# Kernel optimization log

Measured on AMD Instinct MI355X. Metric: run time of the kernel, lower is better.

Reference implementation:

```python
import jax, jax.numpy as jnp
import numpy as np

B, H, S, D = 4, 8, 4096, 64

def setup_inputs() -> dict:
    key = jax.random.key(0)
    kq, kk, kv = jax.random.split(key, 3)
    Q = jax.random.normal(kq, (B, H, S, D), dtype=jnp.float32)
    K = jax.random.normal(kk, (B, H, S, D), dtype=jnp.float32)
    V = jax.random.normal(kv, (B, H, S, D), dtype=jnp.float32)
    return {"Q": Q, "K": K, "V": V}

def reference(Q, K, V):
    scale = 1.0 / jnp.sqrt(jnp.float32(Q.shape[-1]))
    # scores: [B, H, S, S]
    scores = jnp.einsum('bhqd,bhkd->bhqk', Q, K) * scale
    attn = jax.nn.softmax(scores, axis=-1)
    # out: [B, H, S, D]
    return jnp.einsum('bhqk,bhkd->bhqd', attn, V)
```

## Files before the change

kernel.cpp:

```cpp
#include <hip/hip_runtime.h>
#include <hip/hip_bf16.h>

typedef float  f32x16 __attribute__((ext_vector_type(16)));
typedef __bf16 bf16x8 __attribute__((ext_vector_type(8)));
typedef __bf16 bf16x4 __attribute__((ext_vector_type(4)));
typedef __bf16 bf16x2 __attribute__((ext_vector_type(2)));
typedef int    i32x2v __attribute__((ext_vector_type(2)));
typedef int    i32x4v __attribute__((ext_vector_type(4)));

#define SEQ   4096
#define DDIM  64
#define KB    64
#define NT    (SEQ / KB)
#define TILEB 16384
#define WSNEED (32ull * NT * TILEB)
#define SCL   0.18033688011112042f
#define DEFT  16.0f

#if __has_builtin(__builtin_amdgcn_exp2f)
#define EXP2(x) __builtin_amdgcn_exp2f(x)
#else
#define EXP2(x) __expf((x) * 0.6931471805599453f)
#endif

__device__ __forceinline__ int swzb(int row) {
  return (row & 7) ^ ((row >> 3) & 3);
}

__device__ __forceinline__ void pswap32(int &x, int &y) {
#if __has_builtin(__builtin_amdgcn_permlane32_swap)
  i32x2v r = __builtin_amdgcn_permlane32_swap(x, y, false, false);
  x = r[0]; y = r[1];
#else
  asm volatile("v_permlane32_swap_b32 %0, %1" : "+v"(x), "+v"(y));
#endif
}

__device__ __forceinline__ void mfma_acc(f32x16 &acc, bf16x8 a, bf16x8 b) {
  asm("v_mfma_f32_32x32x16_bf16 %0, %1, %2, %0"
      : "+v"(acc) : "v"(a), "v"(b));
}
__device__ __forceinline__ f32x16 mfma_z(bf16x8 a, bf16x8 b) {
  f32x16 d;
  asm("v_mfma_f32_32x32x16_bf16 %0, %1, %2, 0"
      : "=v"(d) : "v"(a), "v"(b));
  return d;
}

__device__ __forceinline__ void gl_lds16(const char* g, char* l) {
  __builtin_amdgcn_global_load_lds(
      (const __attribute__((address_space(1))) void*)g,
      (__attribute__((address_space(3))) void*)l, 16, 0, 0);
}

__device__ __forceinline__ bf16x8 mkfrag(int a, int b, int c, int d) {
  i32x4v v; v[0] = a; v[1] = b; v[2] = c; v[3] = d;
  return __builtin_bit_cast(bf16x8, v);
}

__device__ __forceinline__ float max8(const f32x16& s, int o) {
  float m = fmaxf(fmaxf(s[o+0], s[o+1]), s[o+2]);
  m = fmaxf(fmaxf(m, s[o+3]), s[o+4]);
  m = fmaxf(fmaxf(m, s[o+5]), s[o+6]);
  return fmaxf(m, s[o+7]);
}

__global__ __launch_bounds__(256)
void prep(const float* __restrict__ Kg, const float* __restrict__ Vg,
          char* __restrict__ KVb)
{
  int i = blockIdx.x * 256 + threadIdx.x;
  if (i < (1 << 20)) {
    int row = i >> 3, s_in = i & 7;
    int bh = row >> 12, r = row & 4095, t = r >> 6, kv = r & 63;
    const float* src = Kg + (size_t)row * 64 + s_in * 8;
    float4 f0 = *(const float4*)(src);
    float4 f1 = *(const float4*)(src + 4);
    bf16x8 p;
    p[0] = (__bf16)f0.x; p[1] = (__bf16)f0.y; p[2] = (__bf16)f0.z; p[3] = (__bf16)f0.w;
    p[4] = (__bf16)f1.x; p[5] = (__bf16)f1.y; p[6] = (__bf16)f1.z; p[7] = (__bf16)f1.w;
    char* dst = KVb + (size_t)(bh * NT + t) * TILEB + kv * 128 + ((s_in ^ swzb(kv)) * 16);
    *(bf16x8*)dst = p;
  } else {
    int j = i - (1 << 20);
    int d = j & 63, rest = j >> 6;
    int kvg = rest & 7, t = (rest >> 3) & 63, bh = rest >> 9;
    const float* src = Vg + (size_t)bh * (SEQ * DDIM) + (t * 64 + kvg * 8) * 64 + d;
    bf16x8 p;
    #pragma unroll
    for (int jj = 0; jj < 8; ++jj) p[jj] = (__bf16)src[jj * 64];
    char* dst = KVb + (size_t)(bh * NT + t) * TILEB + 8192 + d * 128
              + ((kvg ^ swzb(d)) * 16);
    *(bf16x8*)dst = p;
  }
}

__global__ __launch_bounds__(512, 4)
void fattn(const float* __restrict__ Qg, const char* __restrict__ KVb,
           float* __restrict__ Og)
{
  __shared__ __align__(16) char smem[2 * TILEB];

  const int tid  = threadIdx.x;
  const int w    = tid >> 6;
  const int lane = tid & 63;
  const int q31  = lane & 31;
  const int h    = lane >> 5;

  int wg = (int)blockIdx.x;
  wg = (wg & 7) * 64 + (wg >> 3);
  const int bh = wg >> 4;
  const int qb = wg & 15;
  const size_t base = (size_t)bh * (SEQ * DDIM);
  const int qrow = qb * 256 + w * 32 + q31;

  bf16x8 aq[4];
  {
    const float* qp = Qg + base + (size_t)qrow * DDIM + 8 * h;
    #pragma unroll
    for (int c = 0; c < 4; ++c) {
      float4 f0 = *(const float4*)(qp + 16 * c);
      float4 f1 = *(const float4*)(qp + 16 * c + 4);
      aq[c][0] = (__bf16)(f0.x * SCL);
      aq[c][1] = (__bf16)(f0.y * SCL);
      aq[c][2] = (__bf16)(f0.z * SCL);
      aq[c][3] = (__bf16)(f0.w * SCL);
      aq[c][4] = (__bf16)(f1.x * SCL);
      aq[c][5] = (__bf16)(f1.y * SCL);
      aq[c][6] = (__bf16)(f1.z * SCL);
      aq[c][7] = (__bf16)(f1.w * SCL);
    }
  }

  const char* kvt = KVb + (size_t)bh * (NT * TILEB);
  const int stg   = w * 1024 + lane * 16;
  const int ldsw  = w * 1024;

  const int swr = swzb(q31) << 4;
  int kaddr[4];
  #pragma unroll
  for (int c = 0; c < 4; ++c)
    kaddr[c] = q31 * 128 + ((32 * c + 16 * h) ^ swr);

  f32x16 o0 = {}, o1 = {};
  float lsum = 0.f;
  int pk[2][8];

#if __has_builtin(__builtin_amdgcn_fdot2_f32_bf16)
  bf16x2 one2; one2[0] = (__bf16)1.0f; one2[1] = (__bf16)1.0f;
#endif

  auto softmax_pack = [&](f32x16& s0, f32x16& s1) {
    #pragma unroll
    for (int r = 0; r < 16; ++r) s0[r] = EXP2(s0[r]);
    #pragma unroll
    for (int r = 0; r < 16; ++r) s1[r] = EXP2(s1[r]);
    #pragma unroll
    for (int u = 0; u < 8; ++u) {
      bf16x2 p0; p0[0] = (__bf16)s0[2*u]; p0[1] = (__bf16)s0[2*u+1];
      pk[0][u] = __builtin_bit_cast(int, p0);
      bf16x2 p1; p1[0] = (__bf16)s1[2*u]; p1[1] = (__bf16)s1[2*u+1];
      pk[1][u] = __builtin_bit_cast(int, p1);
    }
#if __has_builtin(__builtin_amdgcn_fdot2_f32_bf16)
    float a0 = 0.f, a1 = 0.f, a2 = 0.f, a3 = 0.f;
    #pragma unroll
    for (int u = 0; u < 2; ++u) {
      a0 = __builtin_amdgcn_fdot2_f32_bf16(__builtin_bit_cast(bf16x2, pk[0][4*u+0]), one2, a0, false);
      a1 = __builtin_amdgcn_fdot2_f32_bf16(__builtin_bit_cast(bf16x2, pk[0][4*u+1]), one2, a1, false);
      a2 = __builtin_amdgcn_fdot2_f32_bf16(__builtin_bit_cast(bf16x2, pk[0][4*u+2]), one2, a2, false);
      a3 = __builtin_amdgcn_fdot2_f32_bf16(__builtin_bit_cast(bf16x2, pk[0][4*u+3]), one2, a3, false);
      a0 = __builtin_amdgcn_fdot2_f32_bf16(__builtin_bit_cast(bf16x2, pk[1][4*u+0]), one2, a0, false);
      a1 = __builtin_amdgcn_fdot2_f32_bf16(__builtin_bit_cast(bf16x2, pk[1][4*u+1]), one2, a1, false);
      a2 = __builtin_amdgcn_fdot2_f32_bf16(__builtin_bit_cast(bf16x2, pk[1][4*u+2]), one2, a2, false);
      a3 = __builtin_amdgcn_fdot2_f32_bf16(__builtin_bit_cast(bf16x2, pk[1][4*u+3]), one2, a3, false);
    }
    lsum += (a0 + a1) + (a2 + a3);
#else
    f32x16 ts = s0 + s1;
    lsum += ((((ts[0]+ts[1])+(ts[2]+ts[3])) + ((ts[4]+ts[5])+(ts[6]+ts[7])))
          +  (((ts[8]+ts[9])+(ts[10]+ts[11])) + ((ts[12]+ts[13])+(ts[14]+ts[15]))));
#endif
    #pragma unroll
    for (int m = 0; m < 2; ++m) {
      pswap32(pk[m][0], pk[m][2]);
      pswap32(pk[m][1], pk[m][3]);
      pswap32(pk[m][4], pk[m][6]);
      pswap32(pk[m][5], pk[m][7]);
    }
  };

  {
    const char* gp = kvt + stg;
    gl_lds16(gp,        smem + ldsw);
    gl_lds16(gp + 8192, smem + ldsw + 8192);
  }
  __syncthreads();

  for (int t = 0; t < NT; ++t) {
    const int cur  = (t & 1) << 14;
    const int nxtb = cur ^ TILEB;
    const bool more = (t + 1) < NT;

    if (more) {
      const char* gp = kvt + (size_t)(t + 1) * TILEB + stg;
      gl_lds16(gp,        smem + nxtb + ldsw);
      gl_lds16(gp + 8192, smem + nxtb + ldsw + 8192);
    }

    f32x16 s0, s1;
    __builtin_amdgcn_s_setprio(1);
    {
      bf16x8 k0 = *(const bf16x8*)(smem + cur + kaddr[0]);
      bf16x8 k1 = *(const bf16x8*)(smem + cur + kaddr[0] + 4096);
      s0 = mfma_z(k0, aq[0]);
      s1 = mfma_z(k1, aq[0]);
    }
    #pragma unroll
    for (int c = 1; c < 4; ++c) {
      bf16x8 k0 = *(const bf16x8*)(smem + cur + kaddr[c]);
      bf16x8 k1 = *(const bf16x8*)(smem + cur + kaddr[c] + 4096);
      mfma_acc(s0, k0, aq[c]);
      mfma_acc(s1, k1, aq[c]);
    }
    __builtin_amdgcn_s_setprio(0);

    softmax_pack(s0, s1);

    __builtin_amdgcn_s_setprio(1);
    #pragma unroll
    for (int c = 0; c < 4; ++c) {
      bf16x8 bp = mkfrag(pk[c>>1][(c&1)*4+0], pk[c>>1][(c&1)*4+1],
                         pk[c>>1][(c&1)*4+2], pk[c>>1][(c&1)*4+3]);
      bf16x8 v0 = *(const bf16x8*)(smem + cur + kaddr[c] + 8192);
      bf16x8 v1 = *(const bf16x8*)(smem + cur + kaddr[c] + 12288);
      mfma_acc(o0, v0, bp);
      mfma_acc(o1, v1, bp);
    }
    __builtin_amdgcn_s_setprio(0);

    __syncthreads();
  }

  float l = lsum + __shfl_xor(lsum, 32);
  float inv = 1.0f / l;
  float* op = Og + base + (size_t)qrow * DDIM + 4 * h;
  #pragma unroll
  for (int rg = 0; rg < 4; ++rg) {
    float4 st0 = { o0[4*rg+0]*inv, o0[4*rg+1]*inv, o0[4*rg+2]*inv, o0[4*rg+3]*inv };
    *(float4*)(op + 8*rg) = st0;
    float4 st1 = { o1[4*rg+0]*inv, o1[4*rg+1]*inv, o1[4*rg+2]*inv, o1[4*rg+3]*inv };
    *(float4*)(op + 8*rg + 32) = st1;
  }
}

__global__ __launch_bounds__(512)
void fattn_fb(const float* __restrict__ Qg, const float* __restrict__ Kg,
              const float* __restrict__ Vg, float* __restrict__ Og)
{
  __shared__ __align__(16) char smem[32768];
  const int tid  = threadIdx.x;
  const int w    = tid >> 6;
  const int lane = tid & 63;
  const int q31  = lane & 31;
  const int h    = lane >> 5;

  int wg = (int)blockIdx.x;
  wg = (wg & 7) * 64 + (wg >> 3);
  const int bh = wg >> 4;
  const int qb = wg & 15;
  const size_t base = (size_t)bh * (SEQ * DDIM);
  const int qrow = qb * 256 + w * 32 + q31;

  bf16x8 aq[4];
  {
    const float* qp = Qg + base + (size_t)qrow * DDIM + 8 * h;
    #pragma unroll
    for (int c = 0; c < 4; ++c) {
      float4 f0 = *(const float4*)(qp + 16 * c);
      float4 f1 = *(const float4*)(qp + 16 * c + 4);
      aq[c][0] = (__bf16)(f0.x * SCL); aq[c][1] = (__bf16)(f0.y * SCL);
      aq[c][2] = (__bf16)(f0.z * SCL); aq[c][3] = (__bf16)(f0.w * SCL);
      aq[c][4] = (__bf16)(f1.x * SCL); aq[c][5] = (__bf16)(f1.y * SCL);
      aq[c][6] = (__bf16)(f1.z * SCL); aq[c][7] = (__bf16)(f1.w * SCL);
    }
  }

  const int kvA = tid >> 4;
  const int dK  = (tid & 15) * 4;
  const int kw0 = ((kvA * 128 + dK * 2) ^ (swzb(kvA) << 4));
  const int kv0 = (tid >> 4) * 2;
  const int dV  = (tid & 15) * 4;
  int vw[4];
  #pragma unroll
  for (int qq = 0; qq < 4; ++qq)
    vw[qq] = 8192 + (((dV + qq) * 128 + kv0 * 2) ^ (swzb(dV + qq) << 4));
  const float* kptr = Kg + base + (size_t)kvA * DDIM + dK;
  const float* vptr = Vg + base + (size_t)kv0 * DDIM + dV;

  const int swr = swzb(q31) << 4;
  int kaddr[4];
  #pragma unroll
  for (int c = 0; c < 4; ++c)
    kaddr[c] = q31 * 128 + ((32 * c + 16 * h) ^ swr);

  f32x16 o0 = {}, o1 = {};
  float mrow = 0.f, lsum = 0.f;

  {
    float4 ka = *(const float4*)(kptr);
    float4 kb = *(const float4*)(kptr + 32 * DDIM);
    float4 va = *(const float4*)(vptr);
    float4 vb = *(const float4*)(vptr + DDIM);
    bf16x4 pa, pb;
    pa[0]=(__bf16)ka.x; pa[1]=(__bf16)ka.y; pa[2]=(__bf16)ka.z; pa[3]=(__bf16)ka.w;
    pb[0]=(__bf16)kb.x; pb[1]=(__bf16)kb.y; pb[2]=(__bf16)kb.z; pb[3]=(__bf16)kb.w;
    *(bf16x4*)(smem + kw0)            = pa;
    *(bf16x4*)(smem + kw0 + 32 * 128) = pb;
    float va4[4] = {va.x, va.y, va.z, va.w};
    float vb4[4] = {vb.x, vb.y, vb.z, vb.w};
    #pragma unroll
    for (int qq = 0; qq < 4; ++qq) {
      bf16x2 p; p[0] = (__bf16)va4[qq]; p[1] = (__bf16)vb4[qq];
      *(bf16x2*)(smem + vw[qq]) = p;
    }
  }

  int rbase = 0;
  for (int t = 0; t < NT; ++t) {
    __syncthreads();
    const bool more = (t + 1) < NT;
    const float* kpt = kptr + (size_t)(t + 1) * (KB * DDIM);
    const float* vpt = vptr + (size_t)(t + 1) * (KB * DDIM);
    float4 ka = {}, kb = {};
    if (more) { ka = *(const float4*)(kpt); kb = *(const float4*)(kpt + 32 * DDIM); }

    f32x16 s0 = {}, s1 = {};
    #pragma unroll
    for (int c = 0; c < 4; ++c) {
      bf16x8 k0 = *(const bf16x8*)(smem + rbase + kaddr[c]);
      bf16x8 k1 = *(const bf16x8*)(smem + rbase + kaddr[c] + 4096);
      s0 = __builtin_amdgcn_mfma_f32_32x32x16_bf16(k0, aq[c], s0, 0, 0, 0);
      s1 = __builtin_amdgcn_mfma_f32_32x32x16_bf16(k1, aq[c], s1, 0, 0, 0);
    }

    float4 va = {}, vb = {};
    if (more) { va = *(const float4*)(vpt); vb = *(const float4*)(vpt + DDIM); }

    float pm;
    {
      float m0 = max8(s0, 0), m1 = max8(s0, 8);
      float m2 = max8(s1, 0), m3 = max8(s1, 8);
      pm = fmaxf(fmaxf(m0, m1), fmaxf(m2, m3));
    }
    if (!__all(pm <= mrow + DEFT)) {
      float tm = fmaxf(pm, __shfl_xor(pm, 32));
      float mn = fmaxf(mrow, tm);
      float corr = EXP2(mrow - mn);
      o0 *= corr; o1 *= corr; lsum *= corr;
      mrow = mn;
    }
    #pragma unroll
    for (int r = 0; r < 16; ++r) s0[r] = EXP2(s0[r] - mrow);
    #pragma unroll
    for (int r = 0; r < 16; ++r) s1[r] = EXP2(s1[r] - mrow);
    f32x16 ts = s0 + s1;
    lsum += ((((ts[0]+ts[1])+(ts[2]+ts[3])) + ((ts[4]+ts[5])+(ts[6]+ts[7])))
          +  (((ts[8]+ts[9])+(ts[10]+ts[11])) + ((ts[12]+ts[13])+(ts[14]+ts[15]))));

    int pk[2][8];
    #pragma unroll
    for (int u = 0; u < 8; ++u) {
      bf16x2 p0; p0[0] = (__bf16)s0[2*u]; p0[1] = (__bf16)s0[2*u+1];
      pk[0][u] = __builtin_bit_cast(int, p0);
      bf16x2 p1; p1[0] = (__bf16)s1[2*u]; p1[1] = (__bf16)s1[2*u+1];
      pk[1][u] = __builtin_bit_cast(int, p1);
    }
    #pragma unroll
    for (int m = 0; m < 2; ++m) {
      pswap32(pk[m][0], pk[m][2]); pswap32(pk[m][1], pk[m][3]);
      pswap32(pk[m][4], pk[m][6]); pswap32(pk[m][5], pk[m][7]);
    }

    const int wb = rbase ^ 16384;
    if (more) {
      bf16x4 pa, pb;
      pa[0]=(__bf16)ka.x; pa[1]=(__bf16)ka.y; pa[2]=(__bf16)ka.z; pa[3]=(__bf16)ka.w;
      pb[0]=(__bf16)kb.x; pb[1]=(__bf16)kb.y; pb[2]=(__bf16)kb.z; pb[3]=(__bf16)kb.w;
      *(bf16x4*)(smem + wb + kw0)            = pa;
      *(bf16x4*)(smem + wb + kw0 + 32 * 128) = pb;
    }

    #pragma unroll
    for (int c = 0; c < 4; ++c) {
      bf16x8 bp = mkfrag(pk[c>>1][(c&1)*4+0], pk[c>>1][(c&1)*4+1],
                         pk[c>>1][(c&1)*4+2], pk[c>>1][(c&1)*4+3]);
      bf16x8 v0 = *(const bf16x8*)(smem + rbase + kaddr[c] + 8192);
      bf16x8 v1 = *(const bf16x8*)(smem + rbase + kaddr[c] + 12288);
      o0 = __builtin_amdgcn_mfma_f32_32x32x16_bf16(v0, bp, o0, 0, 0, 0);
      o1 = __builtin_amdgcn_mfma_f32_32x32x16_bf16(v1, bp, o1, 0, 0, 0);
    }

    if (more) {
      float va4[4] = {va.x, va.y, va.z, va.w};
      float vb4[4] = {vb.x, vb.y, vb.z, vb.w};
      #pragma unroll
      for (int qq = 0; qq < 4; ++qq) {
        bf16x2 p; p[0] = (__bf16)va4[qq]; p[1] = (__bf16)vb4[qq];
        *(bf16x2*)(smem + wb + vw[qq]) = p;
      }
    }
    rbase ^= 16384;
  }

  float l = lsum + __shfl_xor(lsum, 32);
  float inv = 1.0f / l;
  float* op = Og + base + (size_t)qrow * DDIM + 4 * h;
  #pragma unroll
  for (int rg = 0; rg < 4; ++rg) {
    float4 w0 = { o0[4*rg+0]*inv, o0[4*rg+1]*inv, o0[4*rg+2]*inv, o0[4*rg+3]*inv };
    *(float4*)(op + 8*rg) = w0;
    float4 w1 = { o1[4*rg+0]*inv, o1[4*rg+1]*inv, o1[4*rg+2]*inv, o1[4*rg+3]*inv };
    *(float4*)(op + 8*rg + 32) = w1;
  }
}

extern "C" void kernel_launch(void* const* d_in, const int* in_sizes, int n_in,
                              void* d_out, int out_size, void* d_ws, size_t ws_size,
                              hipStream_t stream) {
  const float* Q = (const float*)d_in[0];
  const float* K = (const float*)d_in[1];
  const float* V = (const float*)d_in[2];
  float* O = (float*)d_out;
  if (ws_size >= WSNEED) {
    prep<<<dim3(8192), dim3(256), 0, stream>>>(K, V, (char*)d_ws);
    fattn<<<dim3(512), dim3(512), 0, stream>>>(Q, (const char*)d_ws, O);
  } else {
    fattn_fb<<<dim3(512), dim3(512), 0, stream>>>(Q, K, V, O);
  }
}
```

Measured before the change: 155.6 us.

## Triple-buffer K/V tiles in LDS with two-ahead async prefetch

Moves the K/V staging from double to triple buffering. Each loop iteration now prefetches the tile two steps ahead, and the full __syncthreads is replaced by a partial vmcnt wait plus a bare s_barrier, so the next tile's loads can stay in flight across iterations. This is meant to hide global-to-LDS latency better. In exchange, LDS use grows from 32KB to 48KB per workgroup, which may limit how many 512-thread blocks fit per CU.

```diff
diff --git a/kernel.cpp b/kernel.cpp
--- a/kernel.cpp
+++ b/kernel.cpp
@@ -99,7 +99,7 @@
 void fattn(const float* __restrict__ Qg, const char* __restrict__ KVb,
            float* __restrict__ Og)
 {
-  __shared__ __align__(16) char smem[2 * TILEB];
+  __shared__ __align__(16) char smem[3 * TILEB];
 
   const int tid  = threadIdx.x;
   const int w    = tid >> 6;
@@ -192,34 +192,37 @@
 
   {
     const char* gp = kvt + stg;
-    gl_lds16(gp,        smem + ldsw);
-    gl_lds16(gp + 8192, smem + ldsw + 8192);
-  }
-  __syncthreads();
+    gl_lds16(gp,                smem + ldsw);
+    gl_lds16(gp + 8192,         smem + ldsw + 8192);
+    gl_lds16(gp + TILEB,        smem + TILEB + ldsw);
+    gl_lds16(gp + TILEB + 8192, smem + TILEB + ldsw + 8192);
+  }
+  asm volatile("s_waitcnt vmcnt(2)" ::: "memory");
+  __builtin_amdgcn_s_barrier();
+
+  int b0 = 0, b1 = TILEB, b2 = 2 * TILEB;
 
   for (int t = 0; t < NT; ++t) {
-    const int cur  = (t & 1) << 14;
-    const int nxtb = cur ^ TILEB;
-    const bool more = (t + 1) < NT;
-
-    if (more) {
-      const char* gp = kvt + (size_t)(t + 1) * TILEB + stg;
-      gl_lds16(gp,        smem + nxtb + ldsw);
-      gl_lds16(gp + 8192, smem + nxtb + ldsw + 8192);
+    const bool issue2 = (t + 2) < NT;
+
+    if (issue2) {
+      const char* gp = kvt + (size_t)(t + 2) * TILEB + stg;
+      gl_lds16(gp,        smem + b2 + ldsw);
+      gl_lds16(gp + 8192, smem + b2 + ldsw + 8192);
     }
 
     f32x16 s0, s1;
     __builtin_amdgcn_s_setprio(1);
     {
-      bf16x8 k0 = *(const bf16x8*)(smem + cur + kaddr[0]);
-      bf16x8 k1 = *(const bf16x8*)(smem + cur + kaddr[0] + 4096);
+      bf16x8 k0 = *(const bf16x8*)(smem + b0 + kaddr[0]);
+      bf16x8 k1 = *(const bf16x8*)(smem + b0 + kaddr[0] + 4096);
       s0 = mfma_z(k0, aq[0]);
       s1 = mfma_z(k1, aq[0]);
     }
     #pragma unroll
     for (int c = 1; c < 4; ++c) {
-      bf16x8 k0 = *(const bf16x8*)(smem + cur + kaddr[c]);
-      bf16x8 k1 = *(const bf16x8*)(smem + cur + kaddr[c] + 4096);
+      bf16x8 k0 = *(const bf16x8*)(smem + b0 + kaddr[c]);
+      bf16x8 k1 = *(const bf16x8*)(smem + b0 + kaddr[c] + 4096);
       mfma_acc(s0, k0, aq[c]);
       mfma_acc(s1, k1, aq[c]);
     }
@@ -232,14 +235,19 @@
     for (int c = 0; c < 4; ++c) {
       bf16x8 bp = mkfrag(pk[c>>1][(c&1)*4+0], pk[c>>1][(c&1)*4+1],
                          pk[c>>1][(c&1)*4+2], pk[c>>1][(c&1)*4+3]);
-      bf16x8 v0 = *(const bf16x8*)(smem + cur + kaddr[c] + 8192);
-      bf16x8 v1 = *(const bf16x8*)(smem + cur + kaddr[c] + 12288);
+      bf16x8 v0 = *(const bf16x8*)(smem + b0 + kaddr[c] + 8192);
+      bf16x8 v1 = *(const bf16x8*)(smem + b0 + kaddr[c] + 12288);
       mfma_acc(o0, v0, bp);
       mfma_acc(o1, v1, bp);
     }
     __builtin_amdgcn_s_setprio(0);
 
-    __syncthreads();
+    if (t + 1 < NT) {
+      if (issue2) asm volatile("s_waitcnt vmcnt(2)" ::: "memory");
+      else        asm volatile("s_waitcnt vmcnt(0)" ::: "memory");
+      __builtin_amdgcn_s_barrier();
+    }
+    int tmp = b0; b0 = b1; b1 = b2; b2 = tmp;
   }
 
   float l = lsum + __shfl_xor(lsum, 32);
```

Result: no change. 157.4 us (+1.1%).
